# Kernel tuning notes

Measured on AMD Instinct MI355X. Metric: run time of the kernel, lower is better.

Reference implementation:

```python
import jax, jax.numpy as jnp
import numpy as np

LAMBDA_G, LAMBDA_F, TAU, MIU_NU_OTHER = 1.938, 1.912, 3.5, 0.19
EPS = 1e-8

B, N, C, D = 8, 1000, 4000, 128  # batch, n_points, n_customers, embed_dim


def setup_inputs() -> dict:
    key = jax.random.key(0)
    ks = jax.random.split(key, 12)
    return {
        "embeddings": jax.random.normal(ks[0], (B, N, D), dtype=jnp.float32),
        "chosen_count": jax.random.randint(ks[1], (B, N), 0, 3, dtype=jnp.int32),
        "u_lj_reg": jax.random.uniform(ks[2], (B, N, C), dtype=jnp.float32),
        "u_lj_food": jax.random.uniform(ks[3], (B, N, C), dtype=jnp.float32),
        "u0": jax.random.uniform(ks[4], (B, C), dtype=jnp.float32),
        "pop": jax.random.uniform(ks[5], (B, C, 1), dtype=jnp.float32),
        "delivery_distances_reg_set": jax.random.uniform(ks[6], (B, N, 1), dtype=jnp.float32),
        "delivery_distances_food_set": jax.random.uniform(ks[7], (B, N, 1), dtype=jnp.float32),
        "fixed_cost_point": jax.random.uniform(ks[8], (B, 1, N), dtype=jnp.float32),
        "W": jax.random.normal(ks[9], (D, D), dtype=jnp.float32) * (1.0 / np.sqrt(D)),
        "b": jax.random.normal(ks[10], (D,), dtype=jnp.float32) * 0.01,
    }


def reference(embeddings, chosen_count, u_lj_reg, u_lj_food, u0, pop,
              delivery_distances_reg_set, delivery_distances_food_set,
              fixed_cost_point, W, b):
    batch_size, n_points = chosen_count.shape
    regular = (chosen_count >= 1).astype(jnp.float32)            # [B,N]
    food = (chosen_count >= 2).astype(jnp.float32)
    reg_cand = 1.0 - regular
    food_cand = regular - food

    # bmm(u^T, diag(mask)) == column-scale: u_reg[b,c,j] = u[b,j,c] * mask[b,j]
    u_reg = jnp.swapaxes(u_lj_reg, 1, 2) * reg_cand[:, None, :]   # [B,C,N]
    P_reg = u0[..., None] + u_reg + EPS
    revenue_g = jnp.sum(pop * (u_reg / P_reg) * LAMBDA_G, axis=1)  # [B,N]

    u_food = jnp.swapaxes(u_lj_food, 1, 2) * food_cand[:, None, :]
    P_food = u0[..., None] + u_food + EPS
    revenue_f = jnp.sum(pop * (u_food / P_food) * LAMBDA_F, axis=1)

    fcp = fixed_cost_point.reshape(batch_size, n_points)
    del_reg = TAU * (reg_cand * delivery_distances_reg_set[..., 0]) / 1000.0
    fix_reg = reg_cand * fcp
    del_food = TAU * (food_cand * delivery_distances_food_set[..., 0]) / 1000.0
    fix_food = food_cand * fcp

    revenue = revenue_g + revenue_f
    delivery = del_reg + del_food
    fixed = fix_reg + fix_food
    labor = 0.075 * revenue
    land = 0.005 * revenue
    advantage = revenue * MIU_NU_OTHER - labor - land - delivery - fixed
    reward_improve = jnp.clip(advantage, 0.0) / 100.0

    loc_best_soft = jax.nn.softmax(reward_improve, axis=-1)       # [B,N]
    context = jnp.einsum('bnd,bn->bd', embeddings, loc_best_soft)  # [B,D]
    return context @ W.T + b
```

## Files before the change

### kernel.cpp

```cpp
#include <hip/hip_runtime.h>

#define LAMBDA_G 1.938f
#define LAMBDA_F 1.912f
#define TAU_C    3.5f
#define EPSV     1e-8f

constexpr int B = 8, N = 1000, C = 4000, D = 128;

__device__ __forceinline__ float waveReduceSum(float v) {
#pragma unroll
    for (int off = 32; off > 0; off >>= 1)
        v += __shfl_down(v, off, 64);
    return v;
}

__device__ __forceinline__ float waveReduceMax(float v) {
#pragma unroll
    for (int off = 32; off > 0; off >>= 1)
        v = fmaxf(v, __shfl_down(v, off, 64));
    return v;
}

__global__ __launch_bounds__(256) void reward_kernel(
    const float* __restrict__ u_reg, const float* __restrict__ u_food,
    const float* __restrict__ u0,    const float* __restrict__ pop,
    const int*   __restrict__ chosen,
    const float* __restrict__ dd_reg, const float* __restrict__ dd_food,
    const float* __restrict__ fcp,   float* __restrict__ reward)
{
    const int bj = blockIdx.x;
    const int b  = bj / N;
    const int t  = threadIdx.x;
    const int cc = chosen[bj];

    if (cc >= 2) {
        if (t == 0) reward[bj] = 0.0f;
        return;
    }

    const float* __restrict__ u    = (cc == 0 ? u_reg : u_food) + (size_t)bj * C;
    const float* __restrict__ u0b  = u0  + (size_t)b * C;
    const float* __restrict__ popb = pop + (size_t)b * C;
    const float  lam = (cc == 0) ? LAMBDA_G : LAMBDA_F;
    const float  dd  = (cc == 0) ? dd_reg[bj] : dd_food[bj];

    float acc = 0.0f;
    const float4* u4  = (const float4*)u;
    const float4* u04 = (const float4*)u0b;
    const float4* p4  = (const float4*)popb;
    for (int c4 = t; c4 < C / 4; c4 += 256) {
        float4 uv = u4[c4];
        float4 ov = u04[c4];
        float4 pv = p4[c4];
        acc += pv.x * uv.x / (ov.x + uv.x + EPSV);
        acc += pv.y * uv.y / (ov.y + uv.y + EPSV);
        acc += pv.z * uv.z / (ov.z + uv.z + EPSV);
        acc += pv.w * uv.w / (ov.w + uv.w + EPSV);
    }

    __shared__ float red[4];
    float ws = waveReduceSum(acc);
    if ((t & 63) == 0) red[t >> 6] = ws;
    __syncthreads();
    if (t == 0) {
        float s       = red[0] + red[1] + red[2] + red[3];
        float revenue = lam * s;
        float delivery = TAU_C * dd * (1.0f / 1000.0f);
        float fixedc   = fcp[bj];
        float adv = revenue * 0.19f - 0.075f * revenue - 0.005f * revenue
                    - delivery - fixedc;
        reward[bj] = fmaxf(adv, 0.0f) * 0.01f;
    }
}

__global__ __launch_bounds__(256) void context_kernel(
    const float* __restrict__ reward, const float* __restrict__ emb,
    const float* __restrict__ Wm,     const float* __restrict__ bias,
    float* __restrict__ out)
{
    const int b = blockIdx.x;
    const int t = threadIdx.x;

    __shared__ float e[N];
    __shared__ float red[4];
    __shared__ float ctx[2][D];

    const float* __restrict__ r = reward + b * N;

    float m = -1e30f;
    for (int j = t; j < N; j += 256) m = fmaxf(m, r[j]);
    m = waveReduceMax(m);
    if ((t & 63) == 0) red[t >> 6] = m;
    __syncthreads();
    const float mx = fmaxf(fmaxf(red[0], red[1]), fmaxf(red[2], red[3]));

    float s = 0.0f;
    for (int j = t; j < N; j += 256) {
        float ev = expf(r[j] - mx);
        e[j] = ev;
        s += ev;
    }
    s = waveReduceSum(s);
    __syncthreads();
    if ((t & 63) == 0) red[t >> 6] = s;
    __syncthreads();
    const float inv = 1.0f / (red[0] + red[1] + red[2] + red[3]);

    const int d    = t & (D - 1);
    const int half = t >> 7;
    const float* __restrict__ eb = emb + (size_t)b * N * D;
    float acc = 0.0f;
    const int j0 = half * (N / 2), j1 = j0 + (N / 2);
    for (int j = j0; j < j1; ++j)
        acc += eb[(size_t)j * D + d] * e[j];
    ctx[half][d] = acc;
    __syncthreads();
    if (t < D) ctx[0][t] = (ctx[0][t] + ctx[1][t]) * inv;
    __syncthreads();

    if (t < D) {
        const float* __restrict__ wr = Wm + t * D;
        float o = bias[t];
        float a = 0.0f;
#pragma unroll 8
        for (int dd = 0; dd < D; ++dd) a += ctx[0][dd] * wr[dd];
        out[b * D + t] = o + a;
    }
}

extern "C" void kernel_launch(void* const* d_in, const int* in_sizes, int n_in,
                              void* d_out, int out_size, void* d_ws, size_t ws_size,
                              hipStream_t stream) {
    const float* emb     = (const float*)d_in[0];
    const int*   chosen  = (const int*)  d_in[1];
    const float* u_reg   = (const float*)d_in[2];
    const float* u_food  = (const float*)d_in[3];
    const float* u0      = (const float*)d_in[4];
    const float* pop     = (const float*)d_in[5];
    const float* dd_reg  = (const float*)d_in[6];
    const float* dd_food = (const float*)d_in[7];
    const float* fcp     = (const float*)d_in[8];
    const float* Wm      = (const float*)d_in[9];
    const float* bias    = (const float*)d_in[10];
    float* out = (float*)d_out;

    float* reward = (float*)d_ws;

    reward_kernel<<<B * N, 256, 0, stream>>>(u_reg, u_food, u0, pop, chosen,
                                             dd_reg, dd_food, fcp, reward);
    context_kernel<<<B, 256, 0, stream>>>(reward, emb, Wm, bias, out);
}
```

Baseline: 286.0 us.

## Split softmax-weighted context reduction across many blocks with partial sums

Replaces the single per-batch context kernel with three kernels: a softmax normalisation pass, a grid of 200 blocks each reducing a slice of embedding rows with float4 loads into partial sums, and a finalize kernel that sums partials and applies the linear layer. This removes the serial 500-row loop on only 8 blocks that underused the GPU. It adds two extra launches and workspace traffic for probabilities and partials.

```diff
diff --git a/kernel.cpp b/kernel.cpp
--- a/kernel.cpp
+++ b/kernel.cpp
@@ -6,6 +6,7 @@
 #define EPSV     1e-8f
 
 constexpr int B = 8, N = 1000, C = 4000, D = 128;
+constexpr int S = 25, RPB = 40, RPT = 5;
 
 __device__ __forceinline__ float waveReduceSum(float v) {
 #pragma unroll
@@ -73,17 +74,14 @@
     }
 }
 
-__global__ __launch_bounds__(256) void context_kernel(
-    const float* __restrict__ reward, const float* __restrict__ emb,
-    const float* __restrict__ Wm,     const float* __restrict__ bias,
-    float* __restrict__ out)
+__global__ __launch_bounds__(256) void softmax_kernel(
+    const float* __restrict__ reward, float* __restrict__ e_out)
 {
     const int b = blockIdx.x;
     const int t = threadIdx.x;
 
     __shared__ float e[N];
     __shared__ float red[4];
-    __shared__ float ctx[2][D];
 
     const float* __restrict__ r = reward + b * N;
 
@@ -106,26 +104,63 @@
     __syncthreads();
     const float inv = 1.0f / (red[0] + red[1] + red[2] + red[3]);
 
-    const int d    = t & (D - 1);
-    const int half = t >> 7;
-    const float* __restrict__ eb = emb + (size_t)b * N * D;
-    float acc = 0.0f;
-    const int j0 = half * (N / 2), j1 = j0 + (N / 2);
-    for (int j = j0; j < j1; ++j)
-        acc += eb[(size_t)j * D + d] * e[j];
-    ctx[half][d] = acc;
+    for (int j = t; j < N; j += 256)
+        e_out[b * N + j] = e[j] * inv;
+}
+
+__global__ __launch_bounds__(256) void ctx_partial_kernel(
+    const float* __restrict__ e, const float* __restrict__ emb,
+    float* __restrict__ partials)
+{
+    const int blk = blockIdx.x;
+    const int b = blk / S, s = blk % S;
+    const int t = threadIdx.x;
+    const int d4 = t & 31;
+    const int rg = t >> 5;
+
+    const float* __restrict__ eb = emb + ((size_t)b * N + s * RPB) * D;
+    const float* __restrict__ ev = e + b * N + s * RPB;
+
+    float4 acc = {0.f, 0.f, 0.f, 0.f};
+#pragma unroll
+    for (int k = 0; k < RPT; ++k) {
+        const int j = rg * RPT + k;
+        const float w = ev[j];
+        const float4 v = ((const float4*)(eb + (size_t)j * D))[d4];
+        acc.x += v.x * w; acc.y += v.y * w; acc.z += v.z * w; acc.w += v.w * w;
+    }
+
+    __shared__ float lds[8][D];
+    *(float4*)&lds[rg][d4 * 4] = acc;
     __syncthreads();
-    if (t < D) ctx[0][t] = (ctx[0][t] + ctx[1][t]) * inv;
+    if (t < D) {
+        float sum = 0.f;
+#pragma unroll
+        for (int g = 0; g < 8; ++g) sum += lds[g][t];
+        partials[((size_t)b * S + s) * D + t] = sum;
+    }
+}
+
+__global__ __launch_bounds__(128) void finalize_kernel(
+    const float* __restrict__ partials, const float* __restrict__ Wm,
+    const float* __restrict__ bias, float* __restrict__ out)
+{
+    const int b = blockIdx.x;
+    const int t = threadIdx.x;
+
+    __shared__ float ctx[D];
+    float sum = 0.f;
+#pragma unroll 5
+    for (int si = 0; si < S; ++si)
+        sum += partials[((size_t)b * S + si) * D + t];
+    ctx[t] = sum;
     __syncthreads();
 
-    if (t < D) {
-        const float* __restrict__ wr = Wm + t * D;
-        float o = bias[t];
-        float a = 0.0f;
+    const float* __restrict__ wr = Wm + t * D;
+    float a = bias[t];
 #pragma unroll 8
-        for (int dd = 0; dd < D; ++dd) a += ctx[0][dd] * wr[dd];
-        out[b * D + t] = o + a;
-    }
+    for (int dd = 0; dd < D; ++dd) a += ctx[dd] * wr[dd];
+    out[b * D + t] = a;
 }
 
 extern "C" void kernel_launch(void* const* d_in, const int* in_sizes, int n_in,
@@ -144,9 +179,13 @@
     const float* bias    = (const float*)d_in[10];
     float* out = (float*)d_out;
 
-    float* reward = (float*)d_ws;
+    float* reward   = (float*)d_ws;
+    float* e_probs  = reward + B * N;
+    float* partials = e_probs + B * N;
 
     reward_kernel<<<B * N, 256, 0, stream>>>(u_reg, u_food, u0, pop, chosen,
                                              dd_reg, dd_food, fcp, reward);
-    context_kernel<<<B, 256, 0, stream>>>(reward, emb, Wm, bias, out);
+    softmax_kernel<<<B, 256, 0, stream>>>(reward, e_probs);
+    ctx_partial_kernel<<<B * S, 256, 0, stream>>>(e_probs, emb, partials);
+    finalize_kernel<<<B, 128, 0, stream>>>(partials, Wm, bias, out);
 }
```

Result: faster. 261.8 us (-8.5%).
